# Kernel tuning notes

Measured on AMD Instinct MI355X. Metric: run time of the kernel, lower is better.

Reference implementation:

```python
import jax, jax.numpy as jnp
import numpy as np

D_MODEL, D_INT, H = 1024, 64, 16
LAMBDA_INIT = 0.8
B, S = 2, 2048
LN_EPS = 1e-5


def setup_inputs() -> dict:
    key = jax.random.key(0)
    ks = jax.random.split(key, 12)
    sd = 0.02
    return {
        "x": jax.random.normal(ks[0], (B, S, D_MODEL), dtype=jnp.float32),
        "lambda_current": jnp.float32(0.5),
        "mask": jnp.ones((B, S), dtype=jnp.int32),
        # stacked per-head params (WQ1/WK1/WV; WQ2/WK2 are unused in source due to bug)
        "wq": sd * jax.random.normal(ks[1], (H, D_MODEL, D_INT), dtype=jnp.float32),
        "bq": sd * jax.random.normal(ks[2], (H, D_INT), dtype=jnp.float32),
        "wk": sd * jax.random.normal(ks[3], (H, D_MODEL, D_INT), dtype=jnp.float32),
        "bk": sd * jax.random.normal(ks[4], (H, D_INT), dtype=jnp.float32),
        "wv": sd * jax.random.normal(ks[5], (H, D_MODEL, 2 * D_INT), dtype=jnp.float32),
        "bv": sd * jax.random.normal(ks[6], (H, 2 * D_INT), dtype=jnp.float32),
        "wo": sd * jax.random.normal(ks[7], (2 * H * D_INT, D_MODEL), dtype=jnp.float32),
        "bo": sd * jax.random.normal(ks[8], (D_MODEL,), dtype=jnp.float32),
        "ln_g": jnp.ones((2 * D_INT,), dtype=jnp.float32),
        "ln_b": jnp.zeros((2 * D_INT,), dtype=jnp.float32),
    }


def reference(x, lambda_current, mask, wq, bq, wk, bk, wv, bv, wo, bo, ln_g, ln_b):
    b, s, d_model = x.shape
    scale = 1.0 / (d_model ** 0.5)  # source divides by sqrt(WQ1.in_features)
    # per-head projections: [H, B, S, d]
    Q = jnp.einsum('bsd,hdk->hbsk', x, wq) + bq[:, None, None, :]
    K = jnp.einsum('bsd,hdk->hbsk', x, wk) + bk[:, None, None, :]
    V = jnp.einsum('bsd,hdv->hbsv', x, wv) + bv[:, None, None, :]
    scores = jnp.einsum('hbsk,hbtk->hbst', Q, K) * scale
    scores = jnp.where(mask[None, :, None, :] == 0, -jnp.inf, scores)
    A1 = jax.nn.softmax(scores, axis=-1)
    # source bug: Q2/K2 reuse WQ1/WK1 => A2 == A1, so A = A1 - lambda*A2 = (1-lambda)*A1
    A = (1.0 - lambda_current) * A1
    out = jnp.einsum('hbst,hbtv->hbsv', A, V)  # [H,B,S,2*D_INT]
    # per-head LayerNorm (shared gamma/beta), then scale by (1 - lambda_init)
    mu = out.mean(-1, keepdims=True)
    var = out.var(-1, keepdims=True)
    out = (out - mu) / jnp.sqrt(var + LN_EPS) * ln_g + ln_b
    out = out * (1.0 - LAMBDA_INIT)
    cat = out.transpose(1, 2, 0, 3).reshape(b, s, -1)  # concat heads on feature dim
    res = cat @ wo + bo
    return (res, A)
```

## Files before the change

kernel.cpp:

```cpp
#include <hip/hip_runtime.h>
#include <hip/hip_bf16.h>

#define DM   1024
#define DI   64
#define H_   16
#define B_   2
#define S_   2048
#define NTOK 4096

typedef unsigned short u16;
typedef unsigned int u32;
typedef __attribute__((ext_vector_type(8))) short s16x8;
typedef __attribute__((ext_vector_type(4))) float f32x4;
typedef __attribute__((ext_vector_type(4))) unsigned int u32x4;
typedef __attribute__((ext_vector_type(4))) unsigned short u16x4;

#define AS1 __attribute__((address_space(1)))
#define AS3 __attribute__((address_space(3)))

static __device__ __forceinline__ u16 f2bf(float f) {
  unsigned int u = __builtin_bit_cast(unsigned int, f);
  unsigned int r = (u + 0x7fffu + ((u >> 16) & 1u)) >> 16;
  return (u16)r;
}

static __device__ __forceinline__ void gload_lds16(const u16* g, u16* l) {
  __builtin_amdgcn_global_load_lds((const AS1 u32*)(const void*)g,
                                   (AS3 u32*)(void*)l, 16, 0, 0);
}


__global__ void k_cvt_x(const float* __restrict__ in, u16* __restrict__ out) {
  int i = (blockIdx.x * 256 + threadIdx.x) * 4;
  float4 v = *(const float4*)&in[i];
  u16x4 o;
  o[0] = f2bf(v.x); o[1] = f2bf(v.y); o[2] = f2bf(v.z); o[3] = f2bf(v.w);
  *(u16x4*)&out[i] = o;
}

__global__ void k_small(const float* __restrict__ bq, const float* __restrict__ bk,
                        const float* __restrict__ bv, const int* __restrict__ mask,
                        float* __restrict__ bc, float* __restrict__ mbias) {
  int t = blockIdx.x * 256 + threadIdx.x;
  if (t < 1024) bc[t] = bq[t];
  else if (t < 2048) bc[t] = bk[t - 1024];
  else if (t < 4096) bc[t] = bv[t - 2048];
  else if (t < 8192) { int i = t - 4096; mbias[i] = mask[i] ? 0.f : -1e38f; }
}

__global__ void k_tr_f2b(const float* __restrict__ in, u16* __restrict__ out, int R, int C) {
  __shared__ float t[32][33];
  const float* src = in + (size_t)blockIdx.z * R * C;
  u16* dst = out + (size_t)blockIdx.z * C * R;
  int r0 = blockIdx.y * 32, c0 = blockIdx.x * 32;
  for (int i = threadIdx.y; i < 32; i += 8)
    t[i][threadIdx.x] = src[(size_t)(r0 + i) * C + c0 + threadIdx.x];
  __syncthreads();
  for (int i = threadIdx.y; i < 32; i += 8)
    dst[(size_t)(c0 + i) * R + r0 + threadIdx.x] = f2bf(t[threadIdx.x][i]);
}

__global__ void k_tr_b2b(const u16* __restrict__ in, u16* __restrict__ out, int R, int C) {
  __shared__ u16 t[32][33];
  const u16* src = in + (size_t)blockIdx.z * R * C;
  u16* dst = out + (size_t)blockIdx.z * C * R;
  int r0 = blockIdx.y * 32, c0 = blockIdx.x * 32;
  for (int i = threadIdx.y; i < 32; i += 8)
    t[i][threadIdx.x] = src[(size_t)(r0 + i) * C + c0 + threadIdx.x];
  __syncthreads();
  for (int i = threadIdx.y; i < 32; i += 8)
    dst[(size_t)(c0 + i) * R + r0 + threadIdx.x] = t[threadIdx.x][i];
}

template<int MODE>
__global__ __launch_bounds__(256)
void k_gemm(const u16* __restrict__ A, const u16* __restrict__ Bt,
            const float* __restrict__ bias, int Kdim,
            u16* __restrict__ q_out, u16* __restrict__ k_out, u16* __restrict__ v_out,
            float* __restrict__ res_out) {
  const int tid = threadIdx.x;
  const int l = tid & 63, w = tid >> 6;
  const int wm = w >> 1, wn = w & 1;
  const int g = l >> 4, lo = l & 15;
  const int m0 = blockIdx.y * 128, n0 = blockIdx.x * 128;
  __shared__ u16 As[128 * 64];
  __shared__ u16 Bs[128 * 64];
  f32x4 acc[4][4] = {};
  for (int kt = 0; kt < Kdim; kt += 64) {
    __syncthreads();
    for (int cid = tid; cid < 1024; cid += 256) {
      int r = cid >> 3, c = (cid & 7) * 8;
      gload_lds16(&A[(size_t)(m0 + r) * Kdim + kt + c], &As[cid * 8]);
      gload_lds16(&Bt[(size_t)(n0 + r) * Kdim + kt + c], &Bs[cid * 8]);
    }
    __syncthreads();
    for (int kc = 0; kc < 64; kc += 32) {
      s16x8 a[4], b[4];
      for (int i = 0; i < 4; i++)
        a[i] = *(const s16x8*)&As[(wm * 64 + i * 16 + lo) * 64 + kc + 8 * g];
      for (int i = 0; i < 4; i++)
        b[i] = *(const s16x8*)&Bs[(wn * 64 + i * 16 + lo) * 64 + kc + 8 * g];
      for (int mi = 0; mi < 4; mi++)
        for (int ni = 0; ni < 4; ni++)
          acc[mi][ni] = __builtin_amdgcn_mfma_f32_16x16x32_bf16(a[mi], b[ni], acc[mi][ni], 0, 0, 0);
    }
  }
  for (int mi = 0; mi < 4; mi++)
    for (int ni = 0; ni < 4; ni++)
      for (int j = 0; j < 4; j++) {
        int m = m0 + wm * 64 + mi * 16 + g * 4 + j;
        int n = n0 + wn * 64 + ni * 16 + lo;
        float v = acc[mi][ni][j] + bias[n];
        if (MODE == 0) {
          int bb = m >> 11, s = m & 2047;
          if (n < 1024) {
            int h = n >> 6, d = n & 63;
            q_out[(((size_t)h * B_ + bb) * S_ + s) * 64 + d] = f2bf(v);
          } else if (n < 2048) {
            int nn = n - 1024; int h = nn >> 6, d = nn & 63;
            k_out[(((size_t)h * B_ + bb) * S_ + s) * 64 + d] = f2bf(v);
          } else {
            int nn = n - 2048; int h = nn >> 7, d = nn & 127;
            v_out[(((size_t)h * B_ + bb) * S_ + s) * 128 + d] = f2bf(v);
          }
        } else {
          res_out[(size_t)m * 1024 + n] = v;
        }
      }
}

__global__ __launch_bounds__(256)
void k_attn(const u16* __restrict__ Qb, const u16* __restrict__ Kb,
            const u16* __restrict__ Vtb, const float* __restrict__ mbias,
            const float* __restrict__ lam_p, const float* __restrict__ ln_g,
            const float* __restrict__ ln_b, float* __restrict__ A_out,
            u16* __restrict__ cat) {
  const int tid = threadIdx.x, l = tid & 63, w = tid >> 6;
  const int g = l >> 4, lo = l & 15;
  const int bid = blockIdx.x;
  const int xcd = bid & 7, idx = bid >> 3;
  const int hb = xcd * 4 + (idx >> 4);
  const int s0 = (idx & 15) * 128;
  const int b = hb & 1, h = hb >> 1;
  const float scale2 = 0.03125f * 1.44269504f;

  __shared__ u16 Ks[2][64 * 72];
  __shared__ u16 Vs[2][128 * 72];
  __shared__ u16 Ps[4][32 * 72];

  const u16* Qhb = Qb + (size_t)hb * S_ * 64;
  const u16* Khb = Kb + (size_t)hb * S_ * 64;
  const u16* Vthb = Vtb + (size_t)hb * 128 * S_;
  const float* mb = mbias + (size_t)b * S_;

  s16x8 q0[2], q1[2];
#pragma unroll
  for (int qh = 0; qh < 2; qh++) {
    const int q = s0 + w * 32 + qh * 16 + lo;
    q0[qh] = *(const s16x8*)&Qhb[(size_t)q * 64 + 8 * g];
    q1[qh] = *(const s16x8*)&Qhb[(size_t)q * 64 + 32 + 8 * g];
  }

  {
#pragma unroll
    for (int i = 0; i < 2; i++) {
      int cid = tid + i * 256;
      int r = cid >> 3, c = (cid & 7) * 8;
      *(u32x4*)&Ks[0][r * 72 + c] = *(const u32x4*)&Khb[(size_t)r * 64 + c];
    }
  }
  __syncthreads();
  float ps[2] = {0.f, 0.f};
  for (int t = 0; t < 32; t++) {
    const int kt = t * 64, buf = t & 1;
    const int ktn = (kt + 64) & (S_ - 1);
    u32x4 kreg[2];
#pragma unroll
    for (int i = 0; i < 2; i++) {
      int cid = tid + i * 256;
      kreg[i] = *(const u32x4*)&Khb[(size_t)(ktn + (cid >> 3)) * 64 + (cid & 7) * 8];
    }
#pragma unroll
    for (int nf = 0; nf < 4; nf++) {
      s16x8 k0 = *(const s16x8*)&Ks[buf][(nf * 16 + lo) * 72 + 8 * g];
      s16x8 k1 = *(const s16x8*)&Ks[buf][(nf * 16 + lo) * 72 + 32 + 8 * g];
      f32x4 m4 = *(const f32x4*)&mb[kt + nf * 16 + g * 4];
#pragma unroll
      for (int qh = 0; qh < 2; qh++) {
        f32x4 z = {};
        z = __builtin_amdgcn_mfma_f32_16x16x32_bf16(k0, q0[qh], z, 0, 0, 0);
        z = __builtin_amdgcn_mfma_f32_16x16x32_bf16(k1, q1[qh], z, 0, 0, 0);
        ps[qh] += __builtin_exp2f(z[0] * scale2 + m4[0]);
        ps[qh] += __builtin_exp2f(z[1] * scale2 + m4[1]);
        ps[qh] += __builtin_exp2f(z[2] * scale2 + m4[2]);
        ps[qh] += __builtin_exp2f(z[3] * scale2 + m4[3]);
      }
    }
#pragma unroll
    for (int i = 0; i < 2; i++) {
      int cid = tid + i * 256;
      *(u32x4*)&Ks[buf ^ 1][(cid >> 3) * 72 + (cid & 7) * 8] = kreg[i];
    }
    __syncthreads();
  }
  float rinv[2];
#pragma unroll
  for (int qh = 0; qh < 2; qh++) {
    ps[qh] += __shfl_xor(ps[qh], 16, 64);
    ps[qh] += __shfl_xor(ps[qh], 32, 64);
    rinv[qh] = (1.0f - lam_p[0]) / ps[qh];
  }

  {
#pragma unroll
    for (int i = 0; i < 4; i++) {
      int cid = tid + i * 256;
      int r = cid >> 3, c = (cid & 7) * 8;
      *(u32x4*)&Vs[0][r * 72 + c] = *(const u32x4*)&Vthb[(size_t)r * S_ + c];
    }
  }
  __syncthreads();

  f32x4 o[8][2] = {};
  for (int t = 0; t < 32; t++) {
    const int kt = t * 64, buf = t & 1;
    u32x4 kreg[2], vreg[4];
    const bool pre = (t < 31);
    if (pre) {
      const int ktn = kt + 64;
#pragma unroll
      for (int i = 0; i < 2; i++) {
        int cid = tid + i * 256;
        kreg[i] = *(const u32x4*)&Khb[(size_t)(ktn + (cid >> 3)) * 64 + (cid & 7) * 8];
      }
#pragma unroll
      for (int i = 0; i < 4; i++) {
        int cid = tid + i * 256;
        vreg[i] = *(const u32x4*)&Vthb[(size_t)(cid >> 3) * S_ + ktn + (cid & 7) * 8];
      }
    }
#pragma unroll
    for (int nf = 0; nf < 4; nf++) {
      s16x8 k0 = *(const s16x8*)&Ks[buf][(nf * 16 + lo) * 72 + 8 * g];
      s16x8 k1 = *(const s16x8*)&Ks[buf][(nf * 16 + lo) * 72 + 32 + 8 * g];
      f32x4 m4 = *(const f32x4*)&mb[kt + nf * 16 + g * 4];
#pragma unroll
      for (int qh = 0; qh < 2; qh++) {
        f32x4 z = {};
        z = __builtin_amdgcn_mfma_f32_16x16x32_bf16(k0, q0[qh], z, 0, 0, 0);
        z = __builtin_amdgcn_mfma_f32_16x16x32_bf16(k1, q1[qh], z, 0, 0, 0);
        f32x4 p4;
        p4[0] = __builtin_exp2f(z[0] * scale2 + m4[0]) * rinv[qh];
        p4[1] = __builtin_exp2f(z[1] * scale2 + m4[1]) * rinv[qh];
        p4[2] = __builtin_exp2f(z[2] * scale2 + m4[2]) * rinv[qh];
        p4[3] = __builtin_exp2f(z[3] * scale2 + m4[3]) * rinv[qh];
        const int q = s0 + w * 32 + qh * 16 + lo;
        __builtin_nontemporal_store(
            p4, (f32x4*)&A_out[((size_t)hb * S_ + q) * S_ + kt + nf * 16 + g * 4]);
        u16x4 pb;
        pb[0] = f2bf(p4[0]); pb[1] = f2bf(p4[1]);
        pb[2] = f2bf(p4[2]); pb[3] = f2bf(p4[3]);
        *(u16x4*)&Ps[w][(qh * 16 + lo) * 72 + nf * 16 + g * 4] = pb;
      }
    }
#pragma unroll
    for (int kc = 0; kc < 2; kc++) {
      s16x8 pa[2];
#pragma unroll
      for (int qh = 0; qh < 2; qh++)
        pa[qh] = *(const s16x8*)&Ps[w][(qh * 16 + lo) * 72 + kc * 32 + 8 * g];
#pragma unroll
      for (int vf = 0; vf < 8; vf++) {
        s16x8 bv = *(const s16x8*)&Vs[buf][(vf * 16 + lo) * 72 + kc * 32 + 8 * g];
#pragma unroll
        for (int qh = 0; qh < 2; qh++)
          o[vf][qh] = __builtin_amdgcn_mfma_f32_16x16x32_bf16(pa[qh], bv, o[vf][qh], 0, 0, 0);
      }
    }
    if (pre) {
#pragma unroll
      for (int i = 0; i < 2; i++) {
        int cid = tid + i * 256;
        *(u32x4*)&Ks[buf ^ 1][(cid >> 3) * 72 + (cid & 7) * 8] = kreg[i];
      }
#pragma unroll
      for (int i = 0; i < 4; i++) {
        int cid = tid + i * 256;
        *(u32x4*)&Vs[buf ^ 1][(cid >> 3) * 72 + (cid & 7) * 8] = vreg[i];
      }
    }
    __syncthreads();
  }

#pragma unroll
  for (int qh = 0; qh < 2; qh++) {
#pragma unroll
    for (int j = 0; j < 4; j++) {
      float sum = 0.f, sq = 0.f;
#pragma unroll
      for (int vf = 0; vf < 8; vf++) { float xv = o[vf][qh][j]; sum += xv; sq += xv * xv; }
      for (int msk = 1; msk < 16; msk <<= 1) {
        sum += __shfl_xor(sum, msk, 64);
        sq += __shfl_xor(sq, msk, 64);
      }
      float mean = sum * (1.f / 128.f);
      float var = sq * (1.f / 128.f) - mean * mean;
      float rstd = rsqrtf(var + 1e-5f);
      int s = s0 + w * 32 + qh * 16 + g * 4 + j;
      u16* cp = cat + ((size_t)(b * S_ + s)) * 2048 + h * 128;
#pragma unroll
      for (int vf = 0; vf < 8; vf++) {
        int c = vf * 16 + lo;
        float y = (o[vf][qh][j] - mean) * rstd * ln_g[c] + ln_b[c];
        cp[c] = f2bf(y * 0.2f);
      }
    }
  }
}


extern "C" void kernel_launch(void* const* d_in, const int* in_sizes, int n_in,
                              void* d_out, int out_size, void* d_ws, size_t ws_size,
                              hipStream_t stream) {
  const float* x    = (const float*)d_in[0];
  const float* lam  = (const float*)d_in[1];
  const int*   mask = (const int*)d_in[2];
  const float* wq   = (const float*)d_in[3];
  const float* bq   = (const float*)d_in[4];
  const float* wk   = (const float*)d_in[5];
  const float* bk   = (const float*)d_in[6];
  const float* wv   = (const float*)d_in[7];
  const float* bv   = (const float*)d_in[8];
  const float* wo   = (const float*)d_in[9];
  const float* bo   = (const float*)d_in[10];
  const float* lng  = (const float*)d_in[11];
  const float* lnb  = (const float*)d_in[12];

  float* res = (float*)d_out;
  float* A   = res + (size_t)NTOK * DM;

  char* ws = (char*)d_ws;
  size_t off = 0;
  auto alloc = [&](size_t bytes) {
    void* p = ws + off;
    off += (bytes + 255) & ~(size_t)255;
    return p;
  };
  u16*   xb    = (u16*)  alloc((size_t)NTOK * DM * 2);
  u16*   Wct   = (u16*)  alloc((size_t)4096 * 1024 * 2);
  float* bc    = (float*)alloc(4096 * 4);
  float* mbias = (float*)alloc(4096 * 4);
  u16*   wot   = (u16*)  alloc((size_t)1024 * 2048 * 2);
  u16*   Qb    = (u16*)  alloc((size_t)32 * S_ * 64 * 2);
  u16*   Kb2   = (u16*)  alloc((size_t)32 * S_ * 64 * 2);
  u16*   Vb    = (u16*)  alloc((size_t)32 * S_ * 128 * 2);
  u16*   Vtb   = (u16*)  alloc((size_t)32 * S_ * 128 * 2);
  u16*   catb  = (u16*)ws;

  k_cvt_x<<<4096, 256, 0, stream>>>(x, xb);
  k_small<<<32, 256, 0, stream>>>(bq, bk, bv, mask, bc, mbias);
  k_tr_f2b<<<dim3(2, 32, 16), dim3(32, 8), 0, stream>>>(wq, Wct, 1024, 64);
  k_tr_f2b<<<dim3(2, 32, 16), dim3(32, 8), 0, stream>>>(wk, Wct + 1024 * 1024, 1024, 64);
  k_tr_f2b<<<dim3(4, 32, 16), dim3(32, 8), 0, stream>>>(wv, Wct + 2048 * 1024, 1024, 128);
  k_tr_f2b<<<dim3(32, 64, 1), dim3(32, 8), 0, stream>>>(wo, wot, 2048, 1024);
  k_gemm<0><<<dim3(32, 32), 256, 0, stream>>>(xb, Wct, bc, 1024, Qb, Kb2, Vb, nullptr);
  k_tr_b2b<<<dim3(4, 64, 32), dim3(32, 8), 0, stream>>>(Vb, Vtb, 2048, 128);
  k_attn<<<dim3(512), 256, 0, stream>>>(Qb, Kb2, Vtb, mbias, lam, lng, lnb, A, catb);
  k_gemm<1><<<dim3(8, 32), 256, 0, stream>>>(catb, wot, bo, 2048, nullptr, nullptr, nullptr, res);
}
```

Measured before the change: 372.2 us.

## Load K directly into registers for softmax-sum pass, drop LDS staging and barriers

The first attention pass, which computes the softmax denominators, now has each wave read its K fragments straight from global memory into double-buffered registers. This replaces staging K through shared memory with a block barrier every tile. The row sums are kept in four separate accumulators to shorten the serial add chain. The second pass swaps __syncthreads for an inline-asm lgkmcnt wait plus s_barrier, issued only when a prefetch was written. The cost is redundant global/L2 reads of K across the four waves and more registers held per thread.

```diff
diff --git a/kernel.cpp b/kernel.cpp
--- a/kernel.cpp
+++ b/kernel.cpp
@@ -27,6 +27,10 @@
 static __device__ __forceinline__ void gload_lds16(const u16* g, u16* l) {
   __builtin_amdgcn_global_load_lds((const AS1 u32*)(const void*)g,
                                    (AS3 u32*)(void*)l, 16, 0, 0);
+}
+
+static __device__ __forceinline__ void lds_barrier() {
+  asm volatile("s_waitcnt lgkmcnt(0)\n\ts_barrier" ::: "memory");
 }
 
 
@@ -161,65 +165,64 @@
     q1[qh] = *(const s16x8*)&Qhb[(size_t)q * 64 + 32 + 8 * g];
   }
 
-  {
-#pragma unroll
-    for (int i = 0; i < 2; i++) {
-      int cid = tid + i * 256;
-      int r = cid >> 3, c = (cid & 7) * 8;
-      *(u32x4*)&Ks[0][r * 72 + c] = *(const u32x4*)&Khb[(size_t)r * 64 + c];
-    }
-  }
-  __syncthreads();
-  float ps[2] = {0.f, 0.f};
+  s16x8 ka[2][4], kb2[2][4];
+#pragma unroll
+  for (int nf = 0; nf < 4; nf++) {
+    const u16* kp = &Khb[(size_t)(nf * 16 + lo) * 64];
+    ka[0][nf]  = *(const s16x8*)&kp[8 * g];
+    kb2[0][nf] = *(const s16x8*)&kp[32 + 8 * g];
+  }
+  f32x4 psv[2] = {};
+#pragma unroll 2
   for (int t = 0; t < 32; t++) {
-    const int kt = t * 64, buf = t & 1;
-    const int ktn = (kt + 64) & (S_ - 1);
-    u32x4 kreg[2];
-#pragma unroll
-    for (int i = 0; i < 2; i++) {
-      int cid = tid + i * 256;
-      kreg[i] = *(const u32x4*)&Khb[(size_t)(ktn + (cid >> 3)) * 64 + (cid & 7) * 8];
-    }
+    const int cur = t & 1;
+    if (t < 31) {
+      const int ktn = (t + 1) * 64;
+#pragma unroll
+      for (int nf = 0; nf < 4; nf++) {
+        const u16* kp = &Khb[(size_t)(ktn + nf * 16 + lo) * 64];
+        ka[cur ^ 1][nf]  = *(const s16x8*)&kp[8 * g];
+        kb2[cur ^ 1][nf] = *(const s16x8*)&kp[32 + 8 * g];
+      }
+    }
+    const int kt = t * 64;
 #pragma unroll
     for (int nf = 0; nf < 4; nf++) {
-      s16x8 k0 = *(const s16x8*)&Ks[buf][(nf * 16 + lo) * 72 + 8 * g];
-      s16x8 k1 = *(const s16x8*)&Ks[buf][(nf * 16 + lo) * 72 + 32 + 8 * g];
       f32x4 m4 = *(const f32x4*)&mb[kt + nf * 16 + g * 4];
 #pragma unroll
       for (int qh = 0; qh < 2; qh++) {
         f32x4 z = {};
-        z = __builtin_amdgcn_mfma_f32_16x16x32_bf16(k0, q0[qh], z, 0, 0, 0);
-        z = __builtin_amdgcn_mfma_f32_16x16x32_bf16(k1, q1[qh], z, 0, 0, 0);
-        ps[qh] += __builtin_exp2f(z[0] * scale2 + m4[0]);
-        ps[qh] += __builtin_exp2f(z[1] * scale2 + m4[1]);
-        ps[qh] += __builtin_exp2f(z[2] * scale2 + m4[2]);
-        ps[qh] += __builtin_exp2f(z[3] * scale2 + m4[3]);
-      }
-    }
-#pragma unroll
-    for (int i = 0; i < 2; i++) {
-      int cid = tid + i * 256;
-      *(u32x4*)&Ks[buf ^ 1][(cid >> 3) * 72 + (cid & 7) * 8] = kreg[i];
-    }
-    __syncthreads();
+        z = __builtin_amdgcn_mfma_f32_16x16x32_bf16(ka[cur][nf], q0[qh], z, 0, 0, 0);
+        z = __builtin_amdgcn_mfma_f32_16x16x32_bf16(kb2[cur][nf], q1[qh], z, 0, 0, 0);
+        psv[qh][0] += __builtin_exp2f(z[0] * scale2 + m4[0]);
+        psv[qh][1] += __builtin_exp2f(z[1] * scale2 + m4[1]);
+        psv[qh][2] += __builtin_exp2f(z[2] * scale2 + m4[2]);
+        psv[qh][3] += __builtin_exp2f(z[3] * scale2 + m4[3]);
+      }
+    }
   }
   float rinv[2];
 #pragma unroll
   for (int qh = 0; qh < 2; qh++) {
-    ps[qh] += __shfl_xor(ps[qh], 16, 64);
-    ps[qh] += __shfl_xor(ps[qh], 32, 64);
-    rinv[qh] = (1.0f - lam_p[0]) / ps[qh];
-  }
-
-  {
-#pragma unroll
-    for (int i = 0; i < 4; i++) {
-      int cid = tid + i * 256;
-      int r = cid >> 3, c = (cid & 7) * 8;
-      *(u32x4*)&Vs[0][r * 72 + c] = *(const u32x4*)&Vthb[(size_t)r * S_ + c];
-    }
-  }
-  __syncthreads();
+    float ps = (psv[qh][0] + psv[qh][1]) + (psv[qh][2] + psv[qh][3]);
+    ps += __shfl_xor(ps, 16, 64);
+    ps += __shfl_xor(ps, 32, 64);
+    rinv[qh] = (1.0f - lam_p[0]) / ps;
+  }
+
+#pragma unroll
+  for (int i = 0; i < 2; i++) {
+    int cid = tid + i * 256;
+    *(u32x4*)&Ks[0][(cid >> 3) * 72 + (cid & 7) * 8] =
+        *(const u32x4*)&Khb[(size_t)(cid >> 3) * 64 + (cid & 7) * 8];
+  }
+#pragma unroll
+  for (int i = 0; i < 4; i++) {
+    int cid = tid + i * 256;
+    *(u32x4*)&Vs[0][(cid >> 3) * 72 + (cid & 7) * 8] =
+        *(const u32x4*)&Vthb[(size_t)(cid >> 3) * S_ + (cid & 7) * 8];
+  }
+  lds_barrier();
 
   f32x4 o[8][2] = {};
   for (int t = 0; t < 32; t++) {
@@ -288,8 +291,8 @@
         int cid = tid + i * 256;
         *(u32x4*)&Vs[buf ^ 1][(cid >> 3) * 72 + (cid & 7) * 8] = vreg[i];
       }
-    }
-    __syncthreads();
+      lds_barrier();
+    }
   }
 
 #pragma unroll
```

Result: slower. 402.2 us (+8.1%).
